# Optimization experiments

Measured on AMD Instinct MI355X. Metric: run time of the kernel, lower is better.

## Reference

```python
import jax, jax.numpy as jnp
import numpy as np

THRESHOLD = 0.5


def setup_inputs() -> dict:
    key = jax.random.key(0)
    T, B = 2048, 4096
    x = jax.random.uniform(key, (T, B, 2), dtype=jnp.float32)  # push/pop signals in [0,1]
    state0 = jnp.zeros((B, 2), dtype=jnp.float32)  # [count, tanh(count)]
    return {"x": x, "state0": state0}


def _step(state, xt):
    # state: [B, 2] = [count, tanh(count)]; xt: [B, 2] = [push, pop]
    push_sig = xt[..., 0]
    pop_sig = xt[..., 1]
    is_push = (push_sig >= THRESHOLD) & (push_sig >= pop_sig)
    is_pop = (pop_sig >= THRESHOLD) & (pop_sig > push_sig)
    delta = jnp.where(is_push, 1.0, jnp.where(is_pop, -1.0, 0.0))
    count = state[..., 0] + delta
    new_state = jnp.stack([count, jnp.tanh(count)], axis=-1)
    return new_state, new_state


def reference(x, state0):
    # x: [T, B, 2], state0: [B, 2] -> all per-step states [T, B, 2]
    _, states = jax.lax.scan(_step, state0, x)
    return states
```

## Files before the change

### kernel.cpp

```cpp
#include <hip/hip_runtime.h>
#include <math.h>

#define T_TOTAL 2048
#define B_TOTAL 4096
#define B2      (B_TOTAL / 2)
#define NCHUNK  64
#define TCHUNK  (T_TOTAL / NCHUNK)

__device__ __forceinline__ int delta_of(float p, float q) {
    return (p >= 0.5f && p >= q) ? 1 : ((q >= 0.5f && q > p) ? -1 : 0);
}

__device__ __forceinline__ float fast_tanh(float x) {
    float e = __builtin_amdgcn_exp2f(x * 2.885390081777927f);
    return 1.0f - 2.0f / (e + 1.0f);
}

__global__ void scan_pass1(const float* __restrict__ x,
                           int* __restrict__ partial,
                           ulonglong2* __restrict__ packed) {
    const int p = blockIdx.x * blockDim.x + threadIdx.x;
    const int c = blockIdx.y;
    const float4* __restrict__ x4 = (const float4*)x;
    const int t0 = c * TCHUNK;

    int s0 = 0, s1 = 0;
    unsigned long long w0 = 0ull, w1 = 0ull;

#pragma unroll
    for (int t = 0; t < 16; ++t) {
        float4 v = x4[(size_t)(t0 + t) * B2 + p];
        int d0 = delta_of(v.x, v.y);
        int d1 = delta_of(v.z, v.w);
        s0 += d0; s1 += d1;
        unsigned int nib = (unsigned int)(d0 & 3) | ((unsigned int)(d1 & 3) << 2);
        w0 |= (unsigned long long)nib << (4 * t);
    }
#pragma unroll
    for (int t = 16; t < 32; ++t) {
        float4 v = x4[(size_t)(t0 + t) * B2 + p];
        int d0 = delta_of(v.x, v.y);
        int d1 = delta_of(v.z, v.w);
        s0 += d0; s1 += d1;
        unsigned int nib = (unsigned int)(d0 & 3) | ((unsigned int)(d1 & 3) << 2);
        w1 |= (unsigned long long)nib << (4 * (t - 16));
    }

    ulonglong2 w; w.x = w0; w.y = w1;
    packed[(size_t)c * B2 + p] = w;
    int2 s; s.x = s0; s.y = s1;
    ((int2*)partial)[(size_t)c * B2 + p] = s;
}

__global__ void scan_pass2(int* __restrict__ partial) {
    const int b = blockIdx.x * blockDim.x + threadIdx.x;
    int off = 0;
#pragma unroll
    for (int c = 0; c < NCHUNK; ++c) {
        int v = partial[(size_t)c * B_TOTAL + b];
        partial[(size_t)c * B_TOTAL + b] = off;
        off += v;
    }
}

__device__ __forceinline__ int sext2(unsigned int bits2) {
    return ((int)(bits2 << 30)) >> 30;
}

__global__ void scan_pass3(const int* __restrict__ partial,
                           const ulonglong2* __restrict__ packed,
                           float* __restrict__ out) {
    const int p = blockIdx.x * blockDim.x + threadIdx.x;
    const int c = blockIdx.y;
    float4* __restrict__ o4 = (float4*)out;
    const int t0 = c * TCHUNK;

    int2 pr = ((const int2*)partial)[(size_t)c * B2 + p];
    int c0 = pr.x, c1 = pr.y;
    ulonglong2 w = packed[(size_t)c * B2 + p];

#pragma unroll
    for (int t = 0; t < 16; ++t) {
        unsigned int nib = (unsigned int)(w.x >> (4 * t)) & 0xFu;
        c0 += sext2(nib & 3u);
        c1 += sext2(nib >> 2);
        float f0 = (float)c0, f1 = (float)c1;
        float4 o; o.x = f0; o.y = fast_tanh(f0); o.z = f1; o.w = fast_tanh(f1);
        o4[(size_t)(t0 + t) * B2 + p] = o;
    }
#pragma unroll
    for (int t = 16; t < 32; ++t) {
        unsigned int nib = (unsigned int)(w.y >> (4 * (t - 16))) & 0xFu;
        c0 += sext2(nib & 3u);
        c1 += sext2(nib >> 2);
        float f0 = (float)c0, f1 = (float)c1;
        float4 o; o.x = f0; o.y = fast_tanh(f0); o.z = f1; o.w = fast_tanh(f1);
        o4[(size_t)(t0 + t) * B2 + p] = o;
    }
}

__global__ void naive_scan(const float* __restrict__ x, float* __restrict__ out) {
    const int b = blockIdx.x * blockDim.x + threadIdx.x;
    if (b >= B_TOTAL) return;
    const float2* __restrict__ x2 = (const float2*)x;
    float2* __restrict__ o2 = (float2*)out;
    int count = 0;
    for (int t = 0; t < T_TOTAL; ++t) {
        float2 v = x2[(size_t)t * B_TOTAL + b];
        count += delta_of(v.x, v.y);
        float fc = (float)count;
        float2 w; w.x = fc; w.y = tanhf(fc);
        o2[(size_t)t * B_TOTAL + b] = w;
    }
}

extern "C" void kernel_launch(void* const* d_in, const int* in_sizes, int n_in,
                              void* d_out, int out_size, void* d_ws, size_t ws_size,
                              hipStream_t stream) {
    const float* x = (const float*)d_in[0];
    float* out = (float*)d_out;

    const size_t partial_bytes = (size_t)NCHUNK * B_TOTAL * sizeof(int);
    const size_t packed_bytes  = (size_t)NCHUNK * B2 * sizeof(ulonglong2);
    if (ws_size < partial_bytes + packed_bytes) {
        naive_scan<<<dim3((B_TOTAL + 255) / 256), dim3(256), 0, stream>>>(x, out);
        return;
    }
    int* partial = (int*)d_ws;
    ulonglong2* packed = (ulonglong2*)((char*)d_ws + partial_bytes);

    dim3 block(256);
    dim3 grid1(B2 / 256, NCHUNK);
    scan_pass1<<<grid1, block, 0, stream>>>(x, partial, packed);
    scan_pass2<<<dim3(B_TOTAL / 256), block, 0, stream>>>(partial);
    scan_pass3<<<grid1, block, 0, stream>>>(partial, packed, out);
}
```

Measured before the change: 115.4 us.

## Fuse three scan passes into one cooperative kernel with grid syncs

Replaces the three-kernel chunked scan with a single cooperative launch of 512 blocks. Each thread keeps its packed deltas in registers across two grid-wide barriers, so the packed workspace write and read are dropped, as are two kernel launch gaps. The middle phase runs the chunk-offset scan using only the first 4096 threads while the rest wait. Pass2 is also changed to load all chunks into registers before storing. The cost is grid-sync overhead and a phase where most of the grid sits idle.

```diff
diff --git a/kernel.cpp b/kernel.cpp
--- a/kernel.cpp
+++ b/kernel.cpp
@@ -1,5 +1,8 @@
 #include <hip/hip_runtime.h>
+#include <hip/hip_cooperative_groups.h>
 #include <math.h>
+
+namespace cg = cooperative_groups;
 
 #define T_TOTAL 2048
 #define B_TOTAL 4096
@@ -14,6 +17,90 @@
 __device__ __forceinline__ float fast_tanh(float x) {
     float e = __builtin_amdgcn_exp2f(x * 2.885390081777927f);
     return 1.0f - 2.0f / (e + 1.0f);
+}
+
+__device__ __forceinline__ int sext2(unsigned int bits2) {
+    return ((int)(bits2 << 30)) >> 30;
+}
+
+__global__ __launch_bounds__(256, 2) void fused_scan(
+        const float* __restrict__ x,
+        float* __restrict__ out,
+        int* __restrict__ partial) {
+    const int tid = threadIdx.x;
+    const int bx  = blockIdx.x;
+    const int c   = bx >> 3;
+    const int p   = ((bx & 7) << 8) | tid;
+    const int t0  = c * TCHUNK;
+    const float4* __restrict__ x4 = (const float4*)x;
+
+    int s0 = 0, s1 = 0;
+    unsigned long long w0 = 0ull, w1 = 0ull;
+
+#pragma unroll
+    for (int t = 0; t < 16; ++t) {
+        float4 v = x4[(size_t)(t0 + t) * B2 + p];
+        int d0 = delta_of(v.x, v.y);
+        int d1 = delta_of(v.z, v.w);
+        s0 += d0; s1 += d1;
+        unsigned int nib = (unsigned int)(d0 & 3) | ((unsigned int)(d1 & 3) << 2);
+        w0 |= (unsigned long long)nib << (4 * t);
+    }
+#pragma unroll
+    for (int t = 16; t < 32; ++t) {
+        float4 v = x4[(size_t)(t0 + t) * B2 + p];
+        int d0 = delta_of(v.x, v.y);
+        int d1 = delta_of(v.z, v.w);
+        s0 += d0; s1 += d1;
+        unsigned int nib = (unsigned int)(d0 & 3) | ((unsigned int)(d1 & 3) << 2);
+        w1 |= (unsigned long long)nib << (4 * (t - 16));
+    }
+
+    int2 s; s.x = s0; s.y = s1;
+    ((int2*)partial)[(size_t)c * B2 + p] = s;
+
+    __threadfence();
+    cg::this_grid().sync();
+
+    const int gtid = (bx << 8) | tid;
+    if (gtid < B_TOTAL) {
+        int v[NCHUNK];
+#pragma unroll
+        for (int cc = 0; cc < NCHUNK; ++cc)
+            v[cc] = partial[cc * B_TOTAL + gtid];
+        int off = 0;
+#pragma unroll
+        for (int cc = 0; cc < NCHUNK; ++cc) { int tmp = v[cc]; v[cc] = off; off += tmp; }
+#pragma unroll
+        for (int cc = 0; cc < NCHUNK; ++cc)
+            partial[cc * B_TOTAL + gtid] = v[cc];
+    }
+
+    __threadfence();
+    cg::this_grid().sync();
+
+    int2 pr = ((const int2*)partial)[(size_t)c * B2 + p];
+    int c0 = pr.x, c1 = pr.y;
+    float4* __restrict__ o4 = (float4*)out;
+
+#pragma unroll
+    for (int t = 0; t < 16; ++t) {
+        unsigned int nib = (unsigned int)(w0 >> (4 * t)) & 0xFu;
+        c0 += sext2(nib & 3u);
+        c1 += sext2(nib >> 2);
+        float f0 = (float)c0, f1 = (float)c1;
+        float4 o; o.x = f0; o.y = fast_tanh(f0); o.z = f1; o.w = fast_tanh(f1);
+        o4[(size_t)(t0 + t) * B2 + p] = o;
+    }
+#pragma unroll
+    for (int t = 16; t < 32; ++t) {
+        unsigned int nib = (unsigned int)(w1 >> (4 * (t - 16))) & 0xFu;
+        c0 += sext2(nib & 3u);
+        c1 += sext2(nib >> 2);
+        float f0 = (float)c0, f1 = (float)c1;
+        float4 o; o.x = f0; o.y = fast_tanh(f0); o.z = f1; o.w = fast_tanh(f1);
+        o4[(size_t)(t0 + t) * B2 + p] = o;
+    }
 }
 
 __global__ void scan_pass1(const float* __restrict__ x,
@@ -54,17 +141,14 @@
 
 __global__ void scan_pass2(int* __restrict__ partial) {
     const int b = blockIdx.x * blockDim.x + threadIdx.x;
+    int v[NCHUNK];
+#pragma unroll
+    for (int cc = 0; cc < NCHUNK; ++cc) v[cc] = partial[cc * B_TOTAL + b];
     int off = 0;
 #pragma unroll
-    for (int c = 0; c < NCHUNK; ++c) {
-        int v = partial[(size_t)c * B_TOTAL + b];
-        partial[(size_t)c * B_TOTAL + b] = off;
-        off += v;
-    }
-}
-
-__device__ __forceinline__ int sext2(unsigned int bits2) {
-    return ((int)(bits2 << 30)) >> 30;
+    for (int cc = 0; cc < NCHUNK; ++cc) { int tmp = v[cc]; v[cc] = off; off += tmp; }
+#pragma unroll
+    for (int cc = 0; cc < NCHUNK; ++cc) partial[cc * B_TOTAL + b] = v[cc];
 }
 
 __global__ void scan_pass3(const int* __restrict__ partial,
@@ -122,6 +206,16 @@
 
     const size_t partial_bytes = (size_t)NCHUNK * B_TOTAL * sizeof(int);
     const size_t packed_bytes  = (size_t)NCHUNK * B2 * sizeof(ulonglong2);
+
+    if (ws_size >= partial_bytes) {
+        int* partial = (int*)d_ws;
+        void* args[] = { (void*)&x, (void*)&out, (void*)&partial };
+        hipError_t err = hipLaunchCooperativeKernel(
+                (const void*)fused_scan, dim3(512), dim3(256), args, 0, stream);
+        if (err == hipSuccess) return;
+        (void)hipGetLastError();
+    }
+
     if (ws_size < partial_bytes + packed_bytes) {
         naive_scan<<<dim3((B_TOTAL + 255) / 256), dim3(256), 0, stream>>>(x, out);
         return;
```

New measurement: 348.2 us. 202% more time.

## Fuse carry scan into output pass and use nontemporal loads/stores

Applied to the files above, without the earlier changes.

Removes the separate serial carry-propagation kernel. Each output block instead sums the preceding chunks' partial counts itself, a redundant scan that is cheap because the partials are small and L2-resident. It also marks the streaming input loads and output stores as nontemporal so they use the cache less. This saves a kernel launch and one dependent pass, at the cost of up to 64 extra small loads per thread in later chunks.

```diff
diff --git a/kernel.cpp b/kernel.cpp
--- a/kernel.cpp
+++ b/kernel.cpp
@@ -6,6 +6,8 @@
 #define B2      (B_TOTAL / 2)
 #define NCHUNK  64
 #define TCHUNK  (T_TOTAL / NCHUNK)
+
+typedef float f32x4 __attribute__((ext_vector_type(4)));
 
 __device__ __forceinline__ int delta_of(float p, float q) {
     return (p >= 0.5f && p >= q) ? 1 : ((q >= 0.5f && q > p) ? -1 : 0);
@@ -16,12 +18,17 @@
     return 1.0f - 2.0f / (e + 1.0f);
 }
 
-__global__ void scan_pass1(const float* __restrict__ x,
-                           int* __restrict__ partial,
-                           ulonglong2* __restrict__ packed) {
+__device__ __forceinline__ int sext2(unsigned int bits2) {
+    return ((int)(bits2 << 30)) >> 30;
+}
+
+__global__ __launch_bounds__(256) void scan_pass1(
+        const float* __restrict__ x,
+        int* __restrict__ partial,
+        ulonglong2* __restrict__ packed) {
     const int p = blockIdx.x * blockDim.x + threadIdx.x;
     const int c = blockIdx.y;
-    const float4* __restrict__ x4 = (const float4*)x;
+    const f32x4* __restrict__ x4 = (const f32x4*)x;
     const int t0 = c * TCHUNK;
 
     int s0 = 0, s1 = 0;
@@ -29,7 +36,7 @@
 
 #pragma unroll
     for (int t = 0; t < 16; ++t) {
-        float4 v = x4[(size_t)(t0 + t) * B2 + p];
+        f32x4 v = __builtin_nontemporal_load(&x4[(size_t)(t0 + t) * B2 + p]);
         int d0 = delta_of(v.x, v.y);
         int d1 = delta_of(v.z, v.w);
         s0 += d0; s1 += d1;
@@ -38,7 +45,7 @@
     }
 #pragma unroll
     for (int t = 16; t < 32; ++t) {
-        float4 v = x4[(size_t)(t0 + t) * B2 + p];
+        f32x4 v = __builtin_nontemporal_load(&x4[(size_t)(t0 + t) * B2 + p]);
         int d0 = delta_of(v.x, v.y);
         int d1 = delta_of(v.z, v.w);
         s0 += d0; s1 += d1;
@@ -52,31 +59,23 @@
     ((int2*)partial)[(size_t)c * B2 + p] = s;
 }
 
-__global__ void scan_pass2(int* __restrict__ partial) {
-    const int b = blockIdx.x * blockDim.x + threadIdx.x;
-    int off = 0;
-#pragma unroll
-    for (int c = 0; c < NCHUNK; ++c) {
-        int v = partial[(size_t)c * B_TOTAL + b];
-        partial[(size_t)c * B_TOTAL + b] = off;
-        off += v;
-    }
-}
-
-__device__ __forceinline__ int sext2(unsigned int bits2) {
-    return ((int)(bits2 << 30)) >> 30;
-}
-
-__global__ void scan_pass3(const int* __restrict__ partial,
-                           const ulonglong2* __restrict__ packed,
-                           float* __restrict__ out) {
+__global__ __launch_bounds__(256) void scan_pass23(
+        const int* __restrict__ partial,
+        const ulonglong2* __restrict__ packed,
+        float* __restrict__ out) {
     const int p = blockIdx.x * blockDim.x + threadIdx.x;
     const int c = blockIdx.y;
-    float4* __restrict__ o4 = (float4*)out;
+    f32x4* __restrict__ o4 = (f32x4*)out;
     const int t0 = c * TCHUNK;
 
-    int2 pr = ((const int2*)partial)[(size_t)c * B2 + p];
-    int c0 = pr.x, c1 = pr.y;
+    int c0 = 0, c1 = 0;
+    const int2* __restrict__ ps = (const int2*)partial;
+#pragma unroll 8
+    for (int cc = 0; cc < c; ++cc) {
+        int2 s = ps[(size_t)cc * B2 + p];
+        c0 += s.x; c1 += s.y;
+    }
+
     ulonglong2 w = packed[(size_t)c * B2 + p];
 
 #pragma unroll
@@ -85,8 +84,8 @@
         c0 += sext2(nib & 3u);
         c1 += sext2(nib >> 2);
         float f0 = (float)c0, f1 = (float)c1;
-        float4 o; o.x = f0; o.y = fast_tanh(f0); o.z = f1; o.w = fast_tanh(f1);
-        o4[(size_t)(t0 + t) * B2 + p] = o;
+        f32x4 o; o.x = f0; o.y = fast_tanh(f0); o.z = f1; o.w = fast_tanh(f1);
+        __builtin_nontemporal_store(o, &o4[(size_t)(t0 + t) * B2 + p]);
     }
 #pragma unroll
     for (int t = 16; t < 32; ++t) {
@@ -94,8 +93,8 @@
         c0 += sext2(nib & 3u);
         c1 += sext2(nib >> 2);
         float f0 = (float)c0, f1 = (float)c1;
-        float4 o; o.x = f0; o.y = fast_tanh(f0); o.z = f1; o.w = fast_tanh(f1);
-        o4[(size_t)(t0 + t) * B2 + p] = o;
+        f32x4 o; o.x = f0; o.y = fast_tanh(f0); o.z = f1; o.w = fast_tanh(f1);
+        __builtin_nontemporal_store(o, &o4[(size_t)(t0 + t) * B2 + p]);
     }
 }
 
@@ -130,8 +129,7 @@
     ulonglong2* packed = (ulonglong2*)((char*)d_ws + partial_bytes);
 
     dim3 block(256);
-    dim3 grid1(B2 / 256, NCHUNK);
-    scan_pass1<<<grid1, block, 0, stream>>>(x, partial, packed);
-    scan_pass2<<<dim3(B_TOTAL / 256), block, 0, stream>>>(partial);
-    scan_pass3<<<grid1, block, 0, stream>>>(partial, packed, out);
+    dim3 grid(B2 / 256, NCHUNK);
+    scan_pass1<<<grid, block, 0, stream>>>(x, partial, packed);
+    scan_pass23<<<grid, block, 0, stream>>>(partial, packed, out);
 }
```

New measurement: 119.3 us. +3.4%, slower.
